# Performance work log

Hardware: AMD Instinct MI355X
Metric: run time of the kernel (lower is better)

## Reference

```python
import jax, jax.numpy as jnp
import numpy as np

N_HEADS = 16

def setup_inputs() -> dict:
    key = jax.random.key(0)
    ks = jax.random.split(key, 5)
    D = 2048
    x = jax.random.normal(ks[0], (2, 2048, D), dtype=jnp.float32)
    scale = 1.0 / np.sqrt(D)
    Wq = jax.random.normal(ks[1], (D, D), dtype=jnp.float32) * scale
    Wk = jax.random.normal(ks[2], (D, D), dtype=jnp.float32) * scale
    Wv = jax.random.normal(ks[3], (D, D), dtype=jnp.float32) * scale
    Wo = jax.random.normal(ks[4], (D, D), dtype=jnp.float32) * scale
    return {"x": x, "Wq": Wq, "Wk": Wk, "Wv": Wv, "Wo": Wo}


def reference(x, Wq, Wk, Wv, Wo):
    # Causal multi-head attention. The original module computes it one query
    # position at a time (recompute loop) but the math is standard causal MHA:
    # query pos attends to key positions 0..pos.
    B, S, D = x.shape
    H = N_HEADS
    hd = D // H
    def split_heads(t):
        return t.reshape(B, S, H, hd).transpose(0, 2, 1, 3)  # (B,H,S,hd)
    q = split_heads(x @ Wq.T)
    k = split_heads(x @ Wk.T)
    v = split_heads(x @ Wv.T)
    scores = jnp.einsum('bhqd,bhkd->bhqk', q, k) / jnp.sqrt(jnp.asarray(hd, x.dtype))
    causal = jnp.tril(jnp.ones((S, S), dtype=bool))  # (S,S), True where allowed
    scores = jnp.where(causal[None, None], scores, jnp.asarray(-jnp.inf, scores.dtype))
    attn = jax.nn.softmax(scores, axis=-1)
    out = jnp.einsum('bhqk,bhkd->bhqd', attn, v)
    out = out.transpose(0, 2, 1, 3).reshape(B, S, D)
    return out @ Wo.T
```

## Files before the change

kernel.cpp:

```cpp
#include <hip/hip_runtime.h>
#include <stdint.h>

#define DD 2048
#define SS 2048
#define NB 2
#define NH 16
#define HDIM 128
#define MM (NB*SS)

typedef __attribute__((ext_vector_type(8))) short bf16x8;
typedef __attribute__((ext_vector_type(4))) float f32x4;
typedef __attribute__((ext_vector_type(4))) ushort u16x4;

__device__ __forceinline__ float fast_exp2(float x) {
  return __builtin_amdgcn_exp2f(x);
}

__device__ __forceinline__ ushort f2bf(float f) {
  union { float f; uint32_t u; } v; v.f = f;
  uint32_t u = v.u;
  return (ushort)((u + 0x7fffu + ((u >> 16) & 1u)) >> 16);
}

__device__ __forceinline__ void gld_lds16(const ushort* g, ushort* l) {
  __builtin_amdgcn_global_load_lds(
      (const __attribute__((address_space(1))) void*)g,
      (__attribute__((address_space(3))) void*)l, 16, 0, 0);
}

__global__ __launch_bounds__(256) void cvt_all(
    const float* __restrict__ x, const float* __restrict__ wq,
    const float* __restrict__ wk, const float* __restrict__ wv,
    const float* __restrict__ wo, ushort* __restrict__ dst)
{
  int i8 = blockIdx.x * 256 + threadIdx.x;
  const int X8 = MM * DD / 8;
  const int W8 = DD * DD / 8;
  const float* src; int off;
  if (i8 < X8)            { src = x;  off = i8; }
  else if (i8 < X8 +   W8){ src = wq; off = i8 - X8; }
  else if (i8 < X8 + 2*W8){ src = wk; off = i8 - (X8 +   W8); }
  else if (i8 < X8 + 3*W8){ src = wv; off = i8 - (X8 + 2*W8); }
  else                    { src = wo; off = i8 - (X8 + 3*W8); }
  const float4* p = (const float4*)src;
  float4 a = p[(long)off*2], b = p[(long)off*2 + 1];
  bf16x8 o;
  o[0]=(short)f2bf(a.x); o[1]=(short)f2bf(a.y); o[2]=(short)f2bf(a.z); o[3]=(short)f2bf(a.w);
  o[4]=(short)f2bf(b.x); o[5]=(short)f2bf(b.y); o[6]=(short)f2bf(b.z); o[7]=(short)f2bf(b.w);
  *(bf16x8*)(dst + (long)i8*8) = o;
}

template<int MODE>
__global__ __launch_bounds__(512, 2) void gemm_pipe(
    const ushort* __restrict__ A, const ushort* __restrict__ Bt,
    ushort* __restrict__ Qo, ushort* __restrict__ Ko, ushort* __restrict__ Vt,
    float* __restrict__ Cf)
{
  __shared__ ushort lds[2 * 24576];
  const int NBX = (MODE == 0) ? 6 : 2;
  const int t = threadIdx.x;
  const int bid = blockIdx.x;
  const int xcd = bid & 7, local = bid >> 3;
  const int bm = local / NBX;
  const int bn = xcd * NBX + (local - bm * NBX);
  const int lane = t & 63;
  const int w = t >> 6;
  const int wr = w >> 1, wcn = w & 1;
  const int lr = lane & 15, lg = lane >> 4;

  int aoff[4], aldo[4], boff[2], bldo[2];
#pragma unroll
  for (int i = 0; i < 4; ++i) {
    int c = i*512 + t, row = c >> 3, slot = c & 7, gc = slot ^ (row & 7);
    aoff[i] = row*DD + gc*8; aldo[i] = c*8;
  }
#pragma unroll
  for (int i = 0; i < 2; ++i) {
    int c = i*512 + t, row = c >> 3, slot = c & 7, gc = slot ^ (row & 7);
    boff[i] = row*DD + gc*8; bldo[i] = 16384 + c*8;
  }
  const ushort* Abase = A  + (long)(bm*256) * DD;
  const ushort* Bbase = Bt + (long)(bn*128) * DD;

#define STAGE(KT, BUF) do {                                   \
    const ushort* a_ = Abase + (KT)*64;                       \
    const ushort* b_ = Bbase + (KT)*64;                       \
    ushort* l_ = lds + (BUF)*24576;                           \
    gld_lds16(a_ + aoff[0], l_ + aldo[0]);                    \
    gld_lds16(a_ + aoff[1], l_ + aldo[1]);                    \
    gld_lds16(a_ + aoff[2], l_ + aldo[2]);                    \
    gld_lds16(a_ + aoff[3], l_ + aldo[3]);                    \
    gld_lds16(b_ + boff[0], l_ + bldo[0]);                    \
    gld_lds16(b_ + boff[1], l_ + bldo[1]);                    \
  } while (0)

  f32x4 acc[4][4] = {};
  const int T = DD / 64;

  STAGE(0, 0);
  STAGE(1, 1);
  asm volatile("s_waitcnt vmcnt(6)" ::: "memory");
  __builtin_amdgcn_sched_barrier(0);
  __builtin_amdgcn_s_barrier();
  __builtin_amdgcn_sched_barrier(0);

  for (int kt = 0; kt < T; ++kt) {
    const char* lb = (const char*)lds + (kt & 1) * 49152;
#pragma unroll
    for (int ks = 0; ks < 2; ++ks) {
      bf16x8 af[4], bfr[4];
#pragma unroll
      for (int m = 0; m < 4; ++m) {
        int row = wr*64 + m*16 + lr;
        af[m] = *(const bf16x8*)(lb + row*128 + (((ks*4 + lg) ^ (row & 7)) * 16));
      }
#pragma unroll
      for (int n = 0; n < 4; ++n) {
        int row = wcn*64 + n*16 + lr;
        bfr[n] = *(const bf16x8*)(lb + 32768 + row*128 + (((ks*4 + lg) ^ (row & 7)) * 16));
      }
      __builtin_amdgcn_s_setprio(1);
#pragma unroll
      for (int m = 0; m < 4; ++m)
#pragma unroll
        for (int n = 0; n < 4; ++n)
          acc[m][n] = __builtin_amdgcn_mfma_f32_16x16x32_bf16(af[m], bfr[n], acc[m][n], 0, 0, 0);
      __builtin_amdgcn_s_setprio(0);
    }
    __builtin_amdgcn_sched_barrier(0);
    __builtin_amdgcn_s_barrier();
    __builtin_amdgcn_sched_barrier(0);
    if (kt + 2 < T) {
      STAGE(kt + 2, kt & 1);
      asm volatile("s_waitcnt vmcnt(6)" ::: "memory");
    } else if (kt + 1 < T) {
      asm volatile("s_waitcnt vmcnt(0)" ::: "memory");
    }
    __builtin_amdgcn_sched_barrier(0);
    __builtin_amdgcn_s_barrier();
    __builtin_amdgcn_sched_barrier(0);
  }
#undef STAGE

  if (MODE == 0) {
    const int region = bn >> 4;
    const int bn2 = bn & 15;
    const int ccb = bn2*128 + wcn*64 + lr;
    const int crb = bm*256 + wr*64 + lg*4;
    if (region < 2) {
      const float scale = (region == 0) ? (0.08838834764831845f * 1.4426950408889634f) : 1.0f;
      ushort* C = (region == 0) ? Qo : Ko;
#pragma unroll
      for (int m = 0; m < 4; ++m)
#pragma unroll
        for (int n = 0; n < 4; ++n)
#pragma unroll
          for (int j = 0; j < 4; ++j)
            C[(long)(crb + m*16 + j) * DD + (ccb + n*16)] = f2bf(acc[m][n][j] * scale);
    } else {
#pragma unroll
      for (int m = 0; m < 4; ++m) {
        int sg = crb + m*16;
        int b2 = sg >> 11, s2 = sg & 2047;
#pragma unroll
        for (int n = 0; n < 4; ++n) {
          int colv = ccb + n*16;
          int h2 = colv >> 7, d2 = colv & 127;
          u16x4 pk;
          pk[0] = f2bf(acc[m][n][0]); pk[1] = f2bf(acc[m][n][1]);
          pk[2] = f2bf(acc[m][n][2]); pk[3] = f2bf(acc[m][n][3]);
          *(u16x4*)(Vt + ((long)((b2*NH + h2)*HDIM + d2)) * SS + s2) = pk;
        }
      }
    }
  } else {
    const int ccb = bn*128 + wcn*64 + lr;
    const int crb = bm*256 + wr*64 + lg*4;
#pragma unroll
    for (int m = 0; m < 4; ++m)
#pragma unroll
      for (int n = 0; n < 4; ++n)
#pragma unroll
        for (int j = 0; j < 4; ++j)
          Cf[(long)(crb + m*16 + j) * DD + (ccb + n*16)] = acc[m][n][j];
  }
}

__global__ __launch_bounds__(512, 4) void attn_fwd(
    const ushort* __restrict__ Qb, const ushort* __restrict__ Kb,
    const ushort* __restrict__ Vtg, ushort* __restrict__ Ob)
{
  __shared__ ushort Ks[64*128];
  __shared__ ushort Vs[128*64];
  __shared__ ushort Ps[8*16*72];

  const int bid = blockIdx.x;
  const int qt = 15 - (bid >> 5);
  const int bh = bid & 31;
  const int b = bh >> 4, h = bh & 15;
  const int t = threadIdx.x;
  const int lane = t & 63;
  const int wq = t >> 6;
  const int lr = lane & 15, lg = lane >> 4;

  const int qbase = qt * 128;
  const long rowQ = (long)(b * SS + qbase + wq * 16);

  bf16x8 qf[4];
#pragma unroll
  for (int c = 0; c < 4; ++c)
    qf[c] = *(const bf16x8*)(Qb + (rowQ + lr) * DD + h*HDIM + c*32 + lg*8);

  f32x4 accO[8] = {};
  float mrow[4], lrow[4];
#pragma unroll
  for (int j = 0; j < 4; ++j) { mrow[j] = -1e30f; lrow[j] = 0.f; }

  const ushort* Kgb = Kb + (long)(b * SS) * DD + h * HDIM;
  const int kr0 = t >> 4, kr1 = 32 + (t >> 4), kci = t & 15;
  const ushort* gk0 = Kgb + (long)kr0 * DD + (kci ^ (kr0 & 7)) * 8;
  const ushort* gk1 = Kgb + (long)kr1 * DD + (kci ^ (kr1 & 7)) * 8;
  ushort* lk0 = Ks + t*8;
  ushort* lk1 = Ks + 4096 + t*8;

  const ushort* Vgb = Vtg + (long)(bh * HDIM) * SS;
  const int vd0 = t >> 3, vd1 = 64 + (t >> 3), vci = t & 7;
  const ushort* gv0 = Vgb + (long)vd0 * SS + (vci ^ (vd0 & 7)) * 8;
  const ushort* gv1 = Vgb + (long)vd1 * SS + (vci ^ (vd1 & 7)) * 8;
  ushort* lv0 = Vs + t*8;
  ushort* lv1 = Vs + 4096 + t*8;

  const int ktmax = 2*qt + 1;
  const int qminw = qbase + wq*16;
  const int qmaxw = qminw + 15;
  ushort* myP = Ps + wq * (16*72);

  for (int kt = 0; kt <= ktmax; ++kt) {
    const int k0 = kt * 64;
    gld_lds16(gk0, lk0); gld_lds16(gk1, lk1);
    gld_lds16(gv0, lv0); gld_lds16(gv1, lv1);
    gk0 += (long)64 * DD; gk1 += (long)64 * DD;
    gv0 += 64; gv1 += 64;
    __syncthreads();

    if (k0 <= qmaxw) {
      f32x4 sc[4] = {};
#pragma unroll
      for (int n = 0; n < 4; ++n) {
        int r = n*16 + lr;
        int swz = (r & 7) << 4;
#pragma unroll
        for (int c = 0; c < 4; ++c) {
          bf16x8 kf = *(const bf16x8*)((const char*)Ks + ((r*256 + c*64 + lg*16) ^ swz));
          sc[n] = __builtin_amdgcn_mfma_f32_16x16x32_bf16(qf[c], kf, sc[n], 0,0,0);
        }
      }
      if (k0 + 63 > qminw) {
#pragma unroll
        for (int n = 0; n < 4; ++n)
#pragma unroll
          for (int j = 0; j < 4; ++j) {
            int kpos = k0 + n*16 + lr;
            int qpos = qminw + lg*4 + j;
            if (kpos > qpos) sc[n][j] = -1e30f;
          }
      }
      float al[4];
#pragma unroll
      for (int j = 0; j < 4; ++j) {
        float tm = fmaxf(fmaxf(sc[0][j], sc[1][j]), fmaxf(sc[2][j], sc[3][j]));
#pragma unroll
        for (int off = 1; off < 16; off <<= 1) tm = fmaxf(tm, __shfl_xor(tm, off));
        float mn = fmaxf(mrow[j], tm);
        float a = fast_exp2(mrow[j] - mn);
        mrow[j] = mn;
        float ts = 0.f;
#pragma unroll
        for (int n = 0; n < 4; ++n) {
          float p = fast_exp2(sc[n][j] - mn);
          sc[n][j] = p; ts += p;
        }
#pragma unroll
        for (int off = 1; off < 16; off <<= 1) ts += __shfl_xor(ts, off);
        lrow[j] = lrow[j] * a + ts;
        al[j] = a;
      }
#pragma unroll
      for (int dg = 0; dg < 8; ++dg) {
        f32x4 v = accO[dg];
        v[0] *= al[0]; v[1] *= al[1]; v[2] *= al[2]; v[3] *= al[3];
        accO[dg] = v;
      }
#pragma unroll
      for (int n = 0; n < 4; ++n)
#pragma unroll
        for (int j = 0; j < 4; ++j)
          myP[(lg*4 + j)*72 + n*16 + lr] = f2bf(sc[n][j]);
      bf16x8 pa0 = *(const bf16x8*)(myP + lr*72 + lg*8);
      bf16x8 pa1 = *(const bf16x8*)(myP + lr*72 + 32 + lg*8);
#pragma unroll
      for (int dg = 0; dg < 8; ++dg) {
        int d = dg*16 + lr;
        int vswz = (d & 7) << 4;
        bf16x8 v0 = *(const bf16x8*)((const char*)Vs + ((d*128 + lg*16) ^ vswz));
        bf16x8 v1 = *(const bf16x8*)((const char*)Vs + ((d*128 + 64 + lg*16) ^ vswz));
        accO[dg] = __builtin_amdgcn_mfma_f32_16x16x32_bf16(pa0, v0, accO[dg], 0,0,0);
        accO[dg] = __builtin_amdgcn_mfma_f32_16x16x32_bf16(pa1, v1, accO[dg], 0,0,0);
      }
    }
    __syncthreads();
  }

  float inv[4];
#pragma unroll
  for (int j = 0; j < 4; ++j) inv[j] = 1.0f / lrow[j];
  ushort* Og = Ob + rowQ * DD + h * HDIM;
#pragma unroll
  for (int dg = 0; dg < 8; ++dg)
#pragma unroll
    for (int j = 0; j < 4; ++j)
      Og[(long)(lg*4 + j) * DD + dg*16 + lr] = f2bf(accO[dg][j] * inv[j]);
}

extern "C" void kernel_launch(void* const* d_in, const int* in_sizes, int n_in,
                              void* d_out, int out_size, void* d_ws, size_t ws_size,
                              hipStream_t stream) {
  const float* x  = (const float*)d_in[0];
  const float* Wq = (const float*)d_in[1];
  const float* Wk = (const float*)d_in[2];
  const float* Wv = (const float*)d_in[3];
  const float* Wo = (const float*)d_in[4];

  ushort* ws  = (ushort*)d_ws;
  ushort* xb  = ws;
  ushort* wqb = ws  + (long)MM*DD;
  ushort* wkb = wqb + (long)DD*DD;
  ushort* wvb = wkb + (long)DD*DD;
  ushort* wob = wvb + (long)DD*DD;
  ushort* Qb  = wob + (long)DD*DD;
  ushort* Kb  = Qb  + (long)MM*DD;
  ushort* Vtg = Kb  + (long)MM*DD;
  (void)wkb; (void)wvb;

  const int CVT_BLOCKS = (MM*DD + 4*DD*DD) / 8 / 256;
  cvt_all<<<CVT_BLOCKS, 256, 0, stream>>>(x, Wq, Wk, Wv, Wo, ws);

  gemm_pipe<0><<<768, 512, 0, stream>>>(xb, wqb, Qb, Kb, Vtg, nullptr);

  attn_fwd<<<512, 512, 0, stream>>>(Qb, Kb, Vtg, xb);

  gemm_pipe<1><<<256, 512, 0, stream>>>(xb, wob, nullptr, nullptr, nullptr,
                                        (float*)d_out);
}
```

Baseline: 278.4 us.

## Restructure GEMM into triple-buffered 8-phase pipeline with interleaved loads

```diff
diff --git a/kernel.cpp b/kernel.cpp
--- a/kernel.cpp
+++ b/kernel.cpp
@@ -51,12 +51,12 @@
 }
 
 template<int MODE>
-__global__ __launch_bounds__(512, 2) void gemm_pipe(
+__global__ __launch_bounds__(512, 2) void gemm8(
     const ushort* __restrict__ A, const ushort* __restrict__ Bt,
     ushort* __restrict__ Qo, ushort* __restrict__ Ko, ushort* __restrict__ Vt,
     float* __restrict__ Cf)
 {
-  __shared__ ushort lds[2 * 24576];
+  __shared__ ushort lds[3 * 24576];
   const int NBX = (MODE == 0) ? 6 : 2;
   const int t = threadIdx.x;
   const int bid = blockIdx.x;
@@ -65,7 +65,8 @@
   const int bn = xcd * NBX + (local - bm * NBX);
   const int lane = t & 63;
   const int w = t >> 6;
-  const int wr = w >> 1, wcn = w & 1;
+  const int wr = w >> 2;
+  const int wcn = w & 3;
   const int lr = lane & 15, lg = lane >> 4;
 
   int aoff[4], aldo[4], boff[2], bldo[2];
@@ -79,91 +80,107 @@
     int c = i*512 + t, row = c >> 3, slot = c & 7, gc = slot ^ (row & 7);
     boff[i] = row*DD + gc*8; bldo[i] = 16384 + c*8;
   }
-  const ushort* Abase = A  + (long)(bm*256) * DD;
-  const ushort* Bbase = Bt + (long)(bn*128) * DD;
-
-#define STAGE(KT, BUF) do {                                   \
-    const ushort* a_ = Abase + (KT)*64;                       \
-    const ushort* b_ = Bbase + (KT)*64;                       \
-    ushort* l_ = lds + (BUF)*24576;                           \
-    gld_lds16(a_ + aoff[0], l_ + aldo[0]);                    \
-    gld_lds16(a_ + aoff[1], l_ + aldo[1]);                    \
-    gld_lds16(a_ + aoff[2], l_ + aldo[2]);                    \
-    gld_lds16(a_ + aoff[3], l_ + aldo[3]);                    \
-    gld_lds16(b_ + boff[0], l_ + bldo[0]);                    \
-    gld_lds16(b_ + boff[1], l_ + bldo[1]);                    \
-  } while (0)
-
-  f32x4 acc[4][4] = {};
+  const ushort* Ab = A  + (long)(bm*256) * DD;
+  const ushort* Bb = Bt + (long)(bn*128) * DD;
+
+#define STG_A01(KT, BUF) do { const ushort* a_ = Ab + (KT)*64;          \
+    ushort* l_ = lds + (BUF)*24576;                                     \
+    gld_lds16(a_ + aoff[0], l_ + aldo[0]);                              \
+    gld_lds16(a_ + aoff[1], l_ + aldo[1]); } while (0)
+#define STG_A23(KT, BUF) do { const ushort* a_ = Ab + (KT)*64;          \
+    ushort* l_ = lds + (BUF)*24576;                                     \
+    gld_lds16(a_ + aoff[2], l_ + aldo[2]);                              \
+    gld_lds16(a_ + aoff[3], l_ + aldo[3]); } while (0)
+#define STG_B(KT, BUF)   do { const ushort* b_ = Bb + (KT)*64;          \
+    ushort* l_ = lds + (BUF)*24576;                                     \
+    gld_lds16(b_ + boff[0], l_ + bldo[0]);                              \
+    gld_lds16(b_ + boff[1], l_ + bldo[1]); } while (0)
+
+#define LDA(dst, m, ks) { int row = wr*128 + (m)*16 + lr;               \
+    (dst) = *(const bf16x8*)(cb + row*128 + ((((ks)*4+lg)^(row&7))*16)); }
+#define LDB(dst, n, ks) { int row = wcn*32 + (n)*16 + lr;               \
+    (dst) = *(const bf16x8*)(cb + 32768 + row*128 + ((((ks)*4+lg)^(row&7))*16)); }
+#define MFMA8(h, av, bv) do {                                           \
+    __builtin_amdgcn_s_setprio(1);                                      \
+    _Pragma("unroll") for (int m = 0; m < 4; ++m)                       \
+      _Pragma("unroll") for (int n = 0; n < 2; ++n)                     \
+        acc[(h)*4+m][n] = __builtin_amdgcn_mfma_f32_16x16x32_bf16(      \
+            av[m], bv[n], acc[(h)*4+m][n], 0, 0, 0);                    \
+    __builtin_amdgcn_s_setprio(0); } while (0)
+#define SB  __builtin_amdgcn_sched_barrier(0)
+#define BAR __builtin_amdgcn_s_barrier()
+#define LGKM0 asm volatile("s_waitcnt lgkmcnt(0)" ::: "memory")
+
+  f32x4 acc[8][2] = {};
   const int T = DD / 64;
 
-  STAGE(0, 0);
-  STAGE(1, 1);
+  STG_A01(0, 0); STG_A23(0, 0); STG_B(0, 0);
+  STG_A01(1, 1); STG_A23(1, 1); STG_B(1, 1);
   asm volatile("s_waitcnt vmcnt(6)" ::: "memory");
-  __builtin_amdgcn_sched_barrier(0);
-  __builtin_amdgcn_s_barrier();
-  __builtin_amdgcn_sched_barrier(0);
-
+  SB; BAR; SB;
+
+  int bcur = 0, bs = 2;
   for (int kt = 0; kt < T; ++kt) {
-    const char* lb = (const char*)lds + (kt & 1) * 49152;
-#pragma unroll
-    for (int ks = 0; ks < 2; ++ks) {
-      bf16x8 af[4], bfr[4];
-#pragma unroll
-      for (int m = 0; m < 4; ++m) {
-        int row = wr*64 + m*16 + lr;
-        af[m] = *(const bf16x8*)(lb + row*128 + (((ks*4 + lg) ^ (row & 7)) * 16));
-      }
-#pragma unroll
-      for (int n = 0; n < 4; ++n) {
-        int row = wcn*64 + n*16 + lr;
-        bfr[n] = *(const bf16x8*)(lb + 32768 + row*128 + (((ks*4 + lg) ^ (row & 7)) * 16));
-      }
-      __builtin_amdgcn_s_setprio(1);
-#pragma unroll
-      for (int m = 0; m < 4; ++m)
-#pragma unroll
-        for (int n = 0; n < 4; ++n)
-          acc[m][n] = __builtin_amdgcn_mfma_f32_16x16x32_bf16(af[m], bfr[n], acc[m][n], 0, 0, 0);
-      __builtin_amdgcn_s_setprio(0);
-    }
-    __builtin_amdgcn_sched_barrier(0);
-    __builtin_amdgcn_s_barrier();
-    __builtin_amdgcn_sched_barrier(0);
-    if (kt + 2 < T) {
-      STAGE(kt + 2, kt & 1);
-      asm volatile("s_waitcnt vmcnt(6)" ::: "memory");
-    } else if (kt + 1 < T) {
-      asm volatile("s_waitcnt vmcnt(0)" ::: "memory");
-    }
-    __builtin_amdgcn_sched_barrier(0);
-    __builtin_amdgcn_s_barrier();
-    __builtin_amdgcn_sched_barrier(0);
-  }
-#undef STAGE
-
+    const char* cb = (const char*)lds + bcur * 49152;
+    const bool st = (kt + 2 < T);
+    bf16x8 a0[4], a1[4], b0[2], b1[2];
+    LDA(a0[0],0,0); LDA(a0[1],1,0); LDA(a0[2],2,0); LDA(a0[3],3,0);
+    LDB(b0[0],0,0); LDB(b0[1],1,0);
+    if (st) STG_A01(kt+2, bs);
+    SB; BAR; LGKM0; SB;
+    MFMA8(0, a0, b0);
+    SB; BAR; SB;
+    LDA(a1[0],4,0); LDA(a1[1],5,0); LDA(a1[2],6,0); LDA(a1[3],7,0);
+    if (st) STG_A23(kt+2, bs);
+    SB; BAR; LGKM0; SB;
+    MFMA8(1, a1, b0);
+    SB; BAR; SB;
+    LDA(a0[0],0,1); LDA(a0[1],1,1); LDA(a0[2],2,1); LDA(a0[3],3,1);
+    LDB(b1[0],0,1); LDB(b1[1],1,1);
+    if (st) STG_B(kt+2, bs);
+    SB; BAR; LGKM0; SB;
+    MFMA8(0, a0, b1);
+    SB; BAR; SB;
+    LDA(a1[0],4,1); LDA(a1[1],5,1); LDA(a1[2],6,1); LDA(a1[3],7,1);
+    if (st) { asm volatile("s_waitcnt vmcnt(6)" ::: "memory"); }
+    else    { asm volatile("s_waitcnt vmcnt(0)" ::: "memory"); }
+    SB; BAR; LGKM0; SB;
+    MFMA8(1, a1, b1);
+    SB; BAR; SB;
+    bcur = (bcur == 2) ? 0 : bcur + 1;
+    bs   = (bs   == 2) ? 0 : bs   + 1;
+  }
+#undef STG_A01
+#undef STG_A23
+#undef STG_B
+#undef LDA
+#undef LDB
+#undef MFMA8
+#undef SB
+#undef BAR
+#undef LGKM0
+
+  const int crb = bm*256 + wr*128 + lg*4;
   if (MODE == 0) {
     const int region = bn >> 4;
-    const int bn2 = bn & 15;
-    const int ccb = bn2*128 + wcn*64 + lr;
-    const int crb = bm*256 + wr*64 + lg*4;
+    const int ccb = (bn & 15)*128 + wcn*32 + lr;
     if (region < 2) {
       const float scale = (region == 0) ? (0.08838834764831845f * 1.4426950408889634f) : 1.0f;
       ushort* C = (region == 0) ? Qo : Ko;
 #pragma unroll
-      for (int m = 0; m < 4; ++m)
-#pragma unroll
-        for (int n = 0; n < 4; ++n)
+      for (int m = 0; m < 8; ++m)
+#pragma unroll
+        for (int n = 0; n < 2; ++n)
 #pragma unroll
           for (int j = 0; j < 4; ++j)
             C[(long)(crb + m*16 + j) * DD + (ccb + n*16)] = f2bf(acc[m][n][j] * scale);
     } else {
 #pragma unroll
-      for (int m = 0; m < 4; ++m) {
+      for (int m = 0; m < 8; ++m) {
         int sg = crb + m*16;
         int b2 = sg >> 11, s2 = sg & 2047;
 #pragma unroll
-        for (int n = 0; n < 4; ++n) {
+        for (int n = 0; n < 2; ++n) {
           int colv = ccb + n*16;
           int h2 = colv >> 7, d2 = colv & 127;
           u16x4 pk;
@@ -174,12 +191,11 @@
       }
     }
   } else {
-    const int ccb = bn*128 + wcn*64 + lr;
-    const int crb = bm*256 + wr*64 + lg*4;
-#pragma unroll
-    for (int m = 0; m < 4; ++m)
-#pragma unroll
-      for (int n = 0; n < 4; ++n)
+    const int ccb = bn*128 + wcn*32 + lr;
+#pragma unroll
+    for (int m = 0; m < 8; ++m)
+#pragma unroll
+      for (int n = 0; n < 2; ++n)
 #pragma unroll
         for (int j = 0; j < 4; ++j)
           Cf[(long)(crb + m*16 + j) * DD + (ccb + n*16)] = acc[m][n][j];
@@ -345,10 +361,10 @@
   const int CVT_BLOCKS = (MM*DD + 4*DD*DD) / 8 / 256;
   cvt_all<<<CVT_BLOCKS, 256, 0, stream>>>(x, Wq, Wk, Wv, Wo, ws);
 
-  gemm_pipe<0><<<768, 512, 0, stream>>>(xb, wqb, Qb, Kb, Vtg, nullptr);
+  gemm8<0><<<768, 512, 0, stream>>>(xb, wqb, Qb, Kb, Vtg, nullptr);
 
   attn_fwd<<<512, 512, 0, stream>>>(Qb, Kb, Vtg, xb);
 
-  gemm_pipe<1><<<256, 512, 0, stream>>>(xb, wob, nullptr, nullptr, nullptr,
-                                        (float*)d_out);
-}
+  gemm8<1><<<256, 512, 0, stream>>>(xb, wob, nullptr, nullptr, nullptr,
+                                    (float*)d_out);
+}
```

Result: no change. 280.5 us (+0.7%).
